# Optimization experiments

Measured on AMD Instinct MI355X. Metric: run time of the kernel, lower is better.

The kernel has to match this reference:

```python
import jax, jax.numpy as jnp
import numpy as np

NUM_HEADS = 4
FEAT_DIM = 128
EMBED_DIM = 128
B, K, C, H, W = 2, 8, 128, 128, 128


def _cross_attn(Qf, Kf, Vf, qw, qb, kw, kb, aqw, aqb, akw, akb):
    """Faithful port of PixelCrossAttentionRefiner._cross_attn.
    Qf: [B, Cq, H, W]; Kf: [B, K, Ck, H, W]; Vf: [B, K, C, H, W].
    Uses only the (head-averaged) softmax weights of MultiheadAttention,
    L2-renormalizes them, then takes a weighted sum of RAW values.
    """
    b, _, h, w = Qf.shape
    k_cand = Kf.shape[1]
    bn = b * h * w
    # Query: per-pixel feature vector -> q1 projection -> attn in-proj (query part)
    Query = jnp.transpose(Qf, (0, 2, 3, 1)).reshape(bn, -1)            # [BN, Cq]
    q = Query @ qw.T + qb                                               # [BN, E]
    # Key: NOTE torch does .permute(0,1,3,4,2).reshape(B*N, K, -1) which is a
    # flat row-major reinterpretation of the (B,K,H,W,Ck) buffer; jnp reshape
    # after transpose has identical semantics, so this is bit-faithful.
    Key = jnp.transpose(Kf, (0, 1, 3, 4, 2)).reshape(bn, k_cand, -1)    # [BN, K, Ck]
    kk = Key @ kw.T + kb                                                # [BN, K, E]
    # nn.MultiheadAttention internal in-projections (value path is dead code)
    qa = q @ aqw.T + aqb                                                # [BN, E]
    ka = kk @ akw.T + akb                                               # [BN, K, E]
    e = qa.shape[-1]
    dh = e // NUM_HEADS
    qh = qa.reshape(bn, NUM_HEADS, dh)
    kh = ka.reshape(bn, k_cand, NUM_HEADS, dh)
    scale = 1.0 / np.sqrt(dh).astype(np.float32)
    scores = jnp.einsum('mhd,mkhd->mhk', qh, kh) * scale                # [BN, H, K]
    attw = jax.nn.softmax(scores, axis=-1).mean(axis=1)                 # avg heads -> [BN, K]
    # F.normalize(p=2, dim=-1, eps=1e-12)
    attw = attw / jnp.maximum(jnp.linalg.norm(attw, axis=-1, keepdims=True), 1e-12)
    Value = jnp.transpose(Vf, (0, 1, 3, 4, 2)).reshape(bn, k_cand, -1)  # [BN, K, C]
    out = jnp.einsum('mk,mkc->mc', attw, Value)                         # [BN, C]
    return jnp.transpose(out.reshape(b, h, w, -1), (0, 3, 1, 2))        # [B, C, H, W]


def _forward(HF_star, HF_cands, Z_cands,
             q1_w, q1_b, k1_w, k1_b, a1_qw, a1_qb, a1_kw, a1_kb,
             q2_w, q2_b, k2_w, k2_b, a2_qw, a2_qb, a2_kw, a2_kb):
    b, c, h, w = HF_star.shape
    k_cand = HF_cands.shape[1]
    i = jnp.linspace(0.0, 1.0, h, dtype=HF_star.dtype)
    j = jnp.linspace(0.0, 1.0, w, dtype=HF_star.dtype)
    ig, jg = jnp.meshgrid(i, j, indexing='ij')
    ig = jnp.broadcast_to(ig[None, None], (b, 1, h, w))
    jg = jnp.broadcast_to(jg[None, None], (b, 1, h, w))
    Q1 = jnp.concatenate([HF_star, ig, jg], axis=1)                     # [B, C+2, H, W]
    ik = jnp.broadcast_to(ig[:, None], (b, k_cand, 1, h, w))
    jk = jnp.broadcast_to(jg[:, None], (b, k_cand, 1, h, w))
    K1 = jnp.concatenate([HF_cands, ik, jk], axis=2)                    # [B, K, C+2, H, W]
    z_star = _cross_attn(Q1, K1, Z_cands, q1_w, q1_b, k1_w, k1_b,
                         a1_qw, a1_qb, a1_kw, a1_kb)                    # [B, C, H, W]
    z_exp = jnp.broadcast_to(z_star[:, None], (b, k_cand, c, h, w))
    Q2 = jnp.concatenate([HF_star, z_star, ig, jg], axis=1)             # [B, 2C+2, H, W]
    K2 = jnp.concatenate([HF_cands, z_exp, ik, jk], axis=2)             # [B, K, 2C+2, H, W]
    z_hat = _cross_attn(Q2, K2, Z_cands, q2_w, q2_b, k2_w, k2_b,
                        a2_qw, a2_qb, a2_kw, a2_kb)
    return z_star, z_hat


def setup_inputs() -> dict:
    key = jax.random.key(0)
    ks = jax.random.split(key, 16)
    E = EMBED_DIM
    d1 = FEAT_DIM + 2
    d2 = 2 * FEAT_DIM + 2

    def lin(k, fan_out, fan_in):
        bound = 1.0 / np.sqrt(fan_in)
        kw, kb = jax.random.split(k)
        return (jax.random.uniform(kw, (fan_out, fan_in), jnp.float32, -bound, bound),
                jax.random.uniform(kb, (fan_out,), jnp.float32, -bound, bound))

    q1_w, q1_b = lin(ks[0], E, d1)
    k1_w, k1_b = lin(ks[1], E, d1)
    q2_w, q2_b = lin(ks[2], E, d2)
    k2_w, k2_b = lin(ks[3], E, d2)
    a1_qw, a1_qb = lin(ks[4], E, E)
    a1_kw, a1_kb = lin(ks[5], E, E)
    a2_qw, a2_qb = lin(ks[6], E, E)
    a2_kw, a2_kb = lin(ks[7], E, E)
    return {
        'HF_star': jax.random.normal(ks[8], (B, C, H, W), jnp.float32),
        'HF_cands': jax.random.normal(ks[9], (B, K, C, H, W), jnp.float32),
        'Z_cands': jax.random.normal(ks[10], (B, K, C, H, W), jnp.float32),
        'q1_w': q1_w, 'q1_b': q1_b, 'k1_w': k1_w, 'k1_b': k1_b,
        'a1_qw': a1_qw, 'a1_qb': a1_qb, 'a1_kw': a1_kw, 'a1_kb': a1_kb,
        'q2_w': q2_w, 'q2_b': q2_b, 'k2_w': k2_w, 'k2_b': k2_b,
        'a2_qw': a2_qw, 'a2_qb': a2_qb, 'a2_kw': a2_kw, 'a2_kb': a2_kb,
    }


def reference(HF_star, HF_cands, Z_cands,
              q1_w, q1_b, k1_w, k1_b, a1_qw, a1_qb, a1_kw, a1_kb,
              q2_w, q2_b, k2_w, k2_b, a2_qw, a2_qb, a2_kw, a2_kb):
    return _forward(HF_star, HF_cands, Z_cands,
                    q1_w, q1_b, k1_w, k1_b, a1_qw, a1_qb, a1_kw, a1_kb,
                    q2_w, q2_b, k2_w, k2_b, a2_qw, a2_qb, a2_kw, a2_kb)
```

## Files before the change

kernel.cpp:

```cpp
#include <hip/hip_runtime.h>
#include <math.h>

constexpr int Bc = 2, Kc = 8, HWc = 16384;
constexpr float SCALE  = 0.17677669529663687f;
constexpr float INV127 = 1.0f / 127.0f;

using short8 = __attribute__((ext_vector_type(8))) short;
using f32x4  = __attribute__((ext_vector_type(4))) float;

constexpr int OWQ1 = 0;
constexpr int OBQ1 = OWQ1 + 130 * 128;
constexpr int OWK1 = OBQ1 + 128;
constexpr int OBK1 = OWK1 + 130 * 128;
constexpr int OWQ2 = OBK1 + 128;
constexpr int OBQ2 = OWQ2 + 258 * 128;
constexpr int OWK2 = OBQ2 + 128;
constexpr int OBK2 = OWK2 + 258 * 128;
constexpr int OPACK = OBK2 + 128;
constexpr int PQ1 = 0;
constexpr int PQ2 = PQ1 + 32 * 512;
constexpr int PY1 = PQ2 + 64 * 512;
constexpr int PY2 = PY1 + 32 * 512;

__device__ __forceinline__ unsigned bfpack(float a, float b) {
    unsigned ua = __float_as_uint(a); ua = (ua + 0x7FFFu + ((ua >> 16) & 1u)) >> 16;
    unsigned ub = __float_as_uint(b); ub = (ub + 0x7FFFu + ((ub >> 16) & 1u)) >> 16;
    return ua | (ub << 16);
}
__device__ __forceinline__ short bf1(float a) {
    unsigned ua = __float_as_uint(a); ua = (ua + 0x7FFFu + ((ua >> 16) & 1u)) >> 16;
    return (short)ua;
}
__device__ __forceinline__ float bflo(unsigned u) { return __uint_as_float(u << 16); }
__device__ __forceinline__ float bfhi(unsigned u) { return __uint_as_float(u & 0xFFFF0000u); }
__device__ __forceinline__ float bf2f(short s) {
    return __uint_as_float(((unsigned)(unsigned short)s) << 16);
}

__global__ __launch_bounds__(128) void prep_kernel(
    const float* __restrict__ q1w, const float* __restrict__ q1b,
    const float* __restrict__ k1w, const float* __restrict__ k1b,
    const float* __restrict__ a1qw, const float* __restrict__ a1qb,
    const float* __restrict__ a1kw, const float* __restrict__ a1kb,
    const float* __restrict__ q2w, const float* __restrict__ q2b,
    const float* __restrict__ k2w, const float* __restrict__ k2b,
    const float* __restrict__ a2qw, const float* __restrict__ a2qb,
    const float* __restrict__ a2kw, const float* __restrict__ a2kb,
    float* __restrict__ ws)
{
    const int job = blockIdx.x / 260;
    const int d   = blockIdx.x % 260;
    const float *aw, *ab, *w, *wb;
    float *owt, *ob;
    int D;
    if (job == 0)      { aw=a1qw; ab=a1qb; w=q1w; wb=q1b; owt=ws+OWQ1; ob=ws+OBQ1; D=130; }
    else if (job == 1) { aw=a1kw; ab=a1kb; w=k1w; wb=k1b; owt=ws+OWK1; ob=ws+OBK1; D=130; }
    else if (job == 2) { aw=a2qw; ab=a2qb; w=q2w; wb=q2b; owt=ws+OWQ2; ob=ws+OBQ2; D=258; }
    else               { aw=a2kw; ab=a2kb; w=k2w; wb=k2b; owt=ws+OWK2; ob=ws+OBK2; D=258; }
    const int e = threadIdx.x;
    if (d < D) {
        float acc = 0.f;
        for (int f = 0; f < 128; ++f) acc += aw[e * 128 + f] * w[f * D + d];
        owt[d * 128 + e] = acc;
    } else if (d == D) {
        float acc = ab[e];
        for (int f = 0; f < 128; ++f) acc += aw[e * 128 + f] * wb[f];
        ob[e] = acc;
    }
}

__global__ __launch_bounds__(64) void pack_kernel(float* __restrict__ ws)
{
    short* pk = (short*)(ws + OPACK);
    const int l = threadIdx.x, bid = blockIdx.x;
    const float* w;
    short* dst;
    short v[8];
    if (bid < 32) {
        const int et = bid >> 2, kt = bid & 3;
        w = ws + OWQ1;
        dst = pk + PQ1 + ((size_t)(et * 4 + kt) * 64 + l) * 8;
        #pragma unroll
        for (int idx = 0; idx < 8; ++idx)
            v[idx] = bf1(w[(kt * 32 + (l >> 4) * 8 + idx) * 128 + et * 16 + (l & 15)]);
    } else if (bid < 96) {
        const int b2 = bid - 32, et = b2 >> 3, kt = b2 & 7;
        w = ws + OWQ2;
        dst = pk + PQ2 + ((size_t)(et * 8 + kt) * 64 + l) * 8;
        #pragma unroll
        for (int idx = 0; idx < 8; ++idx)
            v[idx] = bf1(w[(kt * 32 + (l >> 4) * 8 + idx) * 128 + et * 16 + (l & 15)]);
    } else if (bid < 128) {
        const int b2 = bid - 96, ct = b2 >> 2, h = b2 & 3;
        w = ws + OWK1;
        dst = pk + PY1 + ((size_t)(ct * 4 + h) * 64 + l) * 8;
        #pragma unroll
        for (int idx = 0; idx < 8; ++idx)
            v[idx] = bf1(w[(ct * 16 + (l & 15)) * 128 + h * 32 + (l >> 4) * 8 + idx]);
    } else {
        const int b2 = bid - 128, ct = b2 >> 2, h = b2 & 3;
        w = ws + OWK2;
        dst = pk + PY2 + ((size_t)(ct * 4 + h) * 64 + l) * 8;
        #pragma unroll
        for (int idx = 0; idx < 8; ++idx)
            v[idx] = bf1(w[(ct * 16 + (l & 15)) * 128 + h * 32 + (l >> 4) * 8 + idx]);
    }
    uint4 u;
    u.x = (unsigned)(unsigned short)v[0] | ((unsigned)(unsigned short)v[1] << 16);
    u.y = (unsigned)(unsigned short)v[2] | ((unsigned)(unsigned short)v[3] << 16);
    u.z = (unsigned)(unsigned short)v[4] | ((unsigned)(unsigned short)v[5] << 16);
    u.w = (unsigned)(unsigned short)v[6] | ((unsigned)(unsigned short)v[7] << 16);
    *(uint4*)dst = u;
}

template <int STAGE>
__global__ __launch_bounds__(256) void stage_kernel(
    const float* __restrict__ HFs,
    const float* __restrict__ HFc,
    const float* __restrict__ Zc,
    const float* __restrict__ ws,
    const float* __restrict__ zst,
    float* __restrict__ out)
{
    constexpr int CQ  = (STAGE == 1) ? 128 : 256;
    constexpr int CK  = CQ;
    constexpr int NP  = CK / 128;
    constexpr int NKT = CQ / 32;

    const float* qwt = ws + ((STAGE == 1) ? OWQ1 : OWQ2);
    const float* qb_ = ws + ((STAGE == 1) ? OBQ1 : OBQ2);
    const float* kwt = ws + ((STAGE == 1) ? OWK1 : OWK2);
    const float* kb_ = ws + ((STAGE == 1) ? OBK1 : OBK2);
    const short* pk  = (const short*)(ws + OPACK);
    const short* aQ  = pk + ((STAGE == 1) ? PQ1 : PQ2);
    const short* aY  = pk + ((STAGE == 1) ? PY1 : PY2);

    __shared__ __align__(16) char smem[27136];
    short* sXF = (short*)smem;
    uint2* sYQ = (uint2*)smem;
    short* sQF = (short*)(smem + 17408);
    float* sYX = (float*)(smem + 21504);
    float* sHW = sYX + 192;
    float* sSc = sHW + 576;
    float* sAW = sSc + 512;

    const int t   = threadIdx.x;
    const int l   = t & 63;
    const int wv  = t >> 6;
    const int bid = blockIdx.x;
    const int b   = bid >> 10;
    const int rem = bid & 1023;
    const int ks  = rem >> 7;
    const int hp  = rem & 127;
    const int r0  = ks * 2048 + hp * 16;

    const float ik = (float)hp * INV127;
    const float iq = (float)(r0 >> 7) * INV127;
    const int   w0 = r0 & 127;

    {
        const int q = t & 15, cq = t >> 4;
        #pragma unroll
        for (int r = 0; r < CQ / 64; ++r) {
            const int c0 = cq * 4 + r * 64;
            const float* src = (STAGE == 1 || c0 < 128)
                ? HFs + ((size_t)(b * 128 + c0)) * HWc + r0 + q
                : zst + ((size_t)(b * 128 + (c0 - 128))) * HWc + r0 + q;
            const float x0 = src[0];
            const float x1 = src[(size_t)HWc];
            const float x2 = src[(size_t)2 * HWc];
            const float x3 = src[(size_t)3 * HWc];
            uint2 u; u.x = bfpack(x0, x1); u.y = bfpack(x2, x3);
            const int kt = c0 >> 5, g = (c0 & 31) >> 3, idx0 = c0 & 7;
            *(uint2*)&sXF[kt * 512 + (q + 16 * g) * 8 + idx0] = u;
        }
    }
    __syncthreads();

    {
        const float jqv = (float)(w0 + (l & 15)) * INV127;
        f32x4 acc0, acc1;
        #pragma unroll
        for (int r = 0; r < 4; ++r) {
            const int e0 = (wv * 2 + 0) * 16 + (l >> 4) * 4 + r;
            const int e1 = (wv * 2 + 1) * 16 + (l >> 4) * 4 + r;
            acc0[r] = qb_[e0] + iq * qwt[(size_t)CQ * 128 + e0]
                             + jqv * qwt[(size_t)(CQ + 1) * 128 + e0];
            acc1[r] = qb_[e1] + iq * qwt[(size_t)CQ * 128 + e1]
                             + jqv * qwt[(size_t)(CQ + 1) * 128 + e1];
        }
        #pragma unroll
        for (int kt = 0; kt < NKT; ++kt) {
            const short8 bfr = *(const short8*)&sXF[kt * 512 + l * 8];
            const short8 a0 = *(const short8*)&aQ[(((wv * 2 + 0) * NKT + kt) * 64 + l) * 8];
            const short8 a1 = *(const short8*)&aQ[(((wv * 2 + 1) * NKT + kt) * 64 + l) * 8];
            acc0 = __builtin_amdgcn_mfma_f32_16x16x32_bf16(a0, bfr, acc0, 0, 0, 0);
            acc1 = __builtin_amdgcn_mfma_f32_16x16x32_bf16(a1, bfr, acc1, 0, 0, 0);
        }
        #pragma unroll
        for (int m = 0; m < 2; ++m) {
            const f32x4 a = m ? acc1 : acc0;
            const int e0 = (wv * 2 + m) * 16 + (l >> 4) * 4;
            const int kt = e0 >> 5, g = (e0 & 31) >> 3, idx0 = e0 & 7;
            uint2 u; u.x = bfpack(a[0], a[1]); u.y = bfpack(a[2], a[3]);
            *(uint2*)&sQF[kt * 512 + ((l & 15) + 16 * g) * 8 + idx0] = u;
        }
    }
    __syncthreads();

    if (t < 192) {
        const int q = t & 15, h = (t >> 4) & 3, which = t >> 6;
        const float* wrow = (which == 0) ? kwt + (size_t)CK * 128
                          : (which == 1) ? kwt + (size_t)(CK + 1) * 128
                                         : kb_;
        float acc = 0.f;
        #pragma unroll
        for (int e32 = 0; e32 < 32; ++e32) {
            const int e2 = h * 32 + e32;
            const int g = (e2 & 31) >> 3, idx = e2 & 7;
            acc += wrow[e2] * bf2f(sQF[h * 512 + (q + 16 * g) * 8 + idx]);
        }
        sYX[(which * 4 + h) * 16 + q] = acc;
    }

    short8 bq0 = *(const short8*)&sQF[0 * 512 + l * 8];
    short8 bq1 = *(const short8*)&sQF[1 * 512 + l * 8];
    short8 bq2 = *(const short8*)&sQF[2 * 512 + l * 8];
    short8 bq3 = *(const short8*)&sQF[3 * 512 + l * 8];

    float sacc[4] = {0.f, 0.f, 0.f, 0.f};
    const int pos = t & 127;
    const int ch  = t >> 7;
    const int q   = pos >> 3;
    const f32x4 zf = {0.f, 0.f, 0.f, 0.f};

    #pragma unroll
    for (int p = 0; p < NP; ++p) {
        #pragma unroll
        for (int m = 0; m < 2; ++m) {
            const int ctl = wv * 2 + m;
            const int ct  = p * 8 + ctl;
            f32x4 d0, d1, d2, d3;
            {
                const short8 a0 = *(const short8*)&aY[(((ct * 4) + 0) * 64 + l) * 8];
                const short8 a1 = *(const short8*)&aY[(((ct * 4) + 1) * 64 + l) * 8];
                const short8 a2 = *(const short8*)&aY[(((ct * 4) + 2) * 64 + l) * 8];
                const short8 a3 = *(const short8*)&aY[(((ct * 4) + 3) * 64 + l) * 8];
                d0 = __builtin_amdgcn_mfma_f32_16x16x32_bf16(a0, bq0, zf, 0, 0, 0);
                d1 = __builtin_amdgcn_mfma_f32_16x16x32_bf16(a1, bq1, zf, 0, 0, 0);
                d2 = __builtin_amdgcn_mfma_f32_16x16x32_bf16(a2, bq2, zf, 0, 0, 0);
                d3 = __builtin_amdgcn_mfma_f32_16x16x32_bf16(a3, bq3, zf, 0, 0, 0);
            }
            #pragma unroll
            for (int r = 0; r < 4; ++r) {
                const int cl = ctl * 16 + (l >> 4) * 4 + r;
                uint2 u;
                u.x = bfpack(d0[r], d1[r]);
                u.y = bfpack(d2[r], d3[r]);
                sYQ[cl * 17 + (l & 15)] = u;
            }
        }
        __syncthreads();

        {
            const int cs = p * 128 + ch * 64;
            const float* xp = (STAGE == 1 || cs < 128)
                ? HFc + (((size_t)(b * Kc + ks)) * 128 + cs) * HWc + hp * 128 + pos
                : zst + ((size_t)(b * 128 + (cs - 128))) * HWc + hp * 128 + pos;
            const uint2* yqp = &sYQ[(ch * 64) * 17 + q];
            #pragma unroll 8
            for (int cc = 0; cc < 64; ++cc) {
                const float x = xp[(size_t)cc * HWc];
                const uint2 u = yqp[cc * 17];
                sacc[0] += x * bflo(u.x); sacc[1] += x * bfhi(u.x);
                sacc[2] += x * bflo(u.y); sacc[3] += x * bfhi(u.y);
            }
        }
        __syncthreads();
    }

    if (ch == 1) {
        #pragma unroll
        for (int h = 0; h < 4; ++h) sHW[pos * 4 + h] = sacc[h];
    }
    __syncthreads();
    if (t < 128) {
        const float jk = (float)pos * INV127;
        #pragma unroll
        for (int h = 0; h < 4; ++h) {
            const float s = sacc[h] + sHW[pos * 4 + h]
                          + ik * sYX[(0 * 4 + h) * 16 + q]
                          + jk * sYX[(1 * 4 + h) * 16 + q]
                          +      sYX[(2 * 4 + h) * 16 + q];
            sSc[h * 128 + pos] = s * SCALE;
        }
    }
    __syncthreads();

    if (t < 64) {
        const int qq = t & 15, h = t >> 4;
        float sc[8], m = -INFINITY;
        #pragma unroll
        for (int j = 0; j < 8; ++j) {
            sc[j] = sSc[h * 128 + qq * 8 + j];
            m = fmaxf(m, sc[j]);
        }
        float sum = 0.f;
        #pragma unroll
        for (int j = 0; j < 8; ++j) { sc[j] = __expf(sc[j] - m); sum += sc[j]; }
        const float inv = 0.25f / sum;
        #pragma unroll
        for (int j = 0; j < 8; ++j) sHW[(h * 16 + qq) * 9 + j] = sc[j] * inv;
    }
    __syncthreads();
    if (t < 16) {
        float at[8];
        float n2 = 0.f;
        #pragma unroll
        for (int j = 0; j < 8; ++j) {
            at[j] = sHW[(0 * 16 + t) * 9 + j] + sHW[(1 * 16 + t) * 9 + j]
                  + sHW[(2 * 16 + t) * 9 + j] + sHW[(3 * 16 + t) * 9 + j];
            n2 += at[j] * at[j];
        }
        const float nrm = fmaxf(sqrtf(n2), 1e-12f);
        #pragma unroll
        for (int j = 0; j < 8; ++j) sAW[t * 8 + j] = at[j] / nrm;
    }
    __syncthreads();

    {
        const int idx = t & 15, cg = t >> 4;
        const int c8  = cg * 8;
        const float4 a0 = *(const float4*)&sAW[idx * 8];
        const float4 a1 = *(const float4*)&sAW[idx * 8 + 4];
        const float* zb = Zc + (((size_t)(b * Kc + ks)) * 128 + c8) * HWc + hp * 128 + idx * 8;
        float* ob = out + ((size_t)(b * 128 + c8)) * HWc + r0 + idx;
        #pragma unroll
        for (int i = 0; i < 8; ++i) {
            const float4 z0 = *(const float4*)(zb + (size_t)i * HWc);
            const float4 z1 = *(const float4*)(zb + (size_t)i * HWc + 4);
            ob[(size_t)i * HWc] =
                a0.x * z0.x + a0.y * z0.y + a0.z * z0.z + a0.w * z0.w +
                a1.x * z1.x + a1.y * z1.y + a1.z * z1.z + a1.w * z1.w;
        }
    }
}

extern "C" void kernel_launch(void* const* d_in, const int* in_sizes, int n_in,
                              void* d_out, int out_size, void* d_ws, size_t ws_size,
                              hipStream_t stream)
{
    const float* HFs = (const float*)d_in[0];
    const float* HFc = (const float*)d_in[1];
    const float* Zc  = (const float*)d_in[2];
    float* ws    = (float*)d_ws;
    float* zstar = (float*)d_out;
    float* zhat  = zstar + (size_t)Bc * 128 * HWc;

    prep_kernel<<<1040, 128, 0, stream>>>(
        (const float*)d_in[3],  (const float*)d_in[4],
        (const float*)d_in[5],  (const float*)d_in[6],
        (const float*)d_in[7],  (const float*)d_in[8],
        (const float*)d_in[9],  (const float*)d_in[10],
        (const float*)d_in[11], (const float*)d_in[12],
        (const float*)d_in[13], (const float*)d_in[14],
        (const float*)d_in[15], (const float*)d_in[16],
        (const float*)d_in[17], (const float*)d_in[18],
        ws);

    pack_kernel<<<192, 64, 0, stream>>>(ws);

    stage_kernel<1><<<2048, 256, 0, stream>>>(HFs, HFc, Zc, ws, zstar, zstar);
    stage_kernel<2><<<2048, 256, 0, stream>>>(HFs, HFc, Zc, ws, zstar, zhat);
}
```

Measured before the change: 151.5 us.

## Vectorize feature loads with float4 and register-tile the key-score reduction

The query feature staging now loads float4 along the pixel axis and scatters bf16 values into the MFMA layout, replacing four strided scalar loads per thread. The key-feature dot-product loop is remapped so each thread covers 4 pixels × 4 heads over 16 channels using float4 loads. Partial sums are then combined with a cross-lane shuffle plus a shared-memory reduction across waves. This cuts global load instruction count and improves reuse of each LDS read, at the cost of more registers and extra reduction steps.

```diff
diff --git a/kernel.cpp b/kernel.cpp
--- a/kernel.cpp
+++ b/kernel.cpp
@@ -138,6 +138,7 @@
     __shared__ __align__(16) char smem[27136];
     short* sXF = (short*)smem;
     uint2* sYQ = (uint2*)smem;
+    float* sRed = (float*)smem;
     short* sQF = (short*)(smem + 17408);
     float* sYX = (float*)(smem + 21504);
     float* sHW = sYX + 192;
@@ -159,20 +160,20 @@
     const int   w0 = r0 & 127;
 
     {
-        const int q = t & 15, cq = t >> 4;
+        const int qg = t & 3, c = t >> 2;
         #pragma unroll
         for (int r = 0; r < CQ / 64; ++r) {
-            const int c0 = cq * 4 + r * 64;
-            const float* src = (STAGE == 1 || c0 < 128)
-                ? HFs + ((size_t)(b * 128 + c0)) * HWc + r0 + q
-                : zst + ((size_t)(b * 128 + (c0 - 128))) * HWc + r0 + q;
-            const float x0 = src[0];
-            const float x1 = src[(size_t)HWc];
-            const float x2 = src[(size_t)2 * HWc];
-            const float x3 = src[(size_t)3 * HWc];
-            uint2 u; u.x = bfpack(x0, x1); u.y = bfpack(x2, x3);
-            const int kt = c0 >> 5, g = (c0 & 31) >> 3, idx0 = c0 & 7;
-            *(uint2*)&sXF[kt * 512 + (q + 16 * g) * 8 + idx0] = u;
+            const int cc = c + r * 64;
+            const float* src = (STAGE == 1 || cc < 128)
+                ? HFs + ((size_t)(b * 128 + cc)) * HWc + r0 + qg * 4
+                : zst + ((size_t)(b * 128 + (cc - 128))) * HWc + r0 + qg * 4;
+            const float4 x = *(const float4*)src;
+            const int kt = cc >> 5, g = (cc & 31) >> 3, idx = cc & 7;
+            short* dstb = &sXF[kt * 512 + idx + 16 * g * 8];
+            dstb[(qg * 4 + 0) * 8] = bf1(x.x);
+            dstb[(qg * 4 + 1) * 8] = bf1(x.y);
+            dstb[(qg * 4 + 2) * 8] = bf1(x.z);
+            dstb[(qg * 4 + 3) * 8] = bf1(x.w);
         }
     }
     __syncthreads();
@@ -228,10 +229,14 @@
     short8 bq2 = *(const short8*)&sQF[2 * 512 + l * 8];
     short8 bq3 = *(const short8*)&sQF[3 * 512 + l * 8];
 
-    float sacc[4] = {0.f, 0.f, 0.f, 0.f};
-    const int pos = t & 127;
-    const int ch  = t >> 7;
-    const int q   = pos >> 3;
+    const int pg = t & 31;
+    const int cs = t >> 5;
+    const int q  = pg >> 1;
+    float acc[4][4];
+    #pragma unroll
+    for (int h = 0; h < 4; ++h)
+        #pragma unroll
+        for (int j = 0; j < 4; ++j) acc[h][j] = 0.f;
     const f32x4 zf = {0.f, 0.f, 0.f, 0.f};
 
     #pragma unroll
@@ -263,35 +268,56 @@
         __syncthreads();
 
         {
-            const int cs = p * 128 + ch * 64;
-            const float* xp = (STAGE == 1 || cs < 128)
-                ? HFc + (((size_t)(b * Kc + ks)) * 128 + cs) * HWc + hp * 128 + pos
-                : zst + ((size_t)(b * 128 + (cs - 128))) * HWc + hp * 128 + pos;
-            const uint2* yqp = &sYQ[(ch * 64) * 17 + q];
+            const int cbase = p * 128 + cs * 16;
+            const float* xp = (STAGE == 1 || cbase < 128)
+                ? HFc + (((size_t)(b * Kc + ks)) * 128 + cbase) * HWc + hp * 128 + pg * 4
+                : zst + ((size_t)(b * 128 + (cbase - 128))) * HWc + hp * 128 + pg * 4;
+            const uint2* yqp = &sYQ[(cs * 16) * 17 + q];
             #pragma unroll 8
-            for (int cc = 0; cc < 64; ++cc) {
-                const float x = xp[(size_t)cc * HWc];
+            for (int cc = 0; cc < 16; ++cc) {
+                const float4 x = *(const float4*)(xp + (size_t)cc * HWc);
                 const uint2 u = yqp[cc * 17];
-                sacc[0] += x * bflo(u.x); sacc[1] += x * bfhi(u.x);
-                sacc[2] += x * bflo(u.y); sacc[3] += x * bfhi(u.y);
+                const float y0 = bflo(u.x), y1 = bfhi(u.x);
+                const float y2 = bflo(u.y), y3 = bfhi(u.y);
+                acc[0][0] += y0 * x.x; acc[0][1] += y0 * x.y;
+                acc[0][2] += y0 * x.z; acc[0][3] += y0 * x.w;
+                acc[1][0] += y1 * x.x; acc[1][1] += y1 * x.y;
+                acc[1][2] += y1 * x.z; acc[1][3] += y1 * x.w;
+                acc[2][0] += y2 * x.x; acc[2][1] += y2 * x.y;
+                acc[2][2] += y2 * x.z; acc[2][3] += y2 * x.w;
+                acc[3][0] += y3 * x.x; acc[3][1] += y3 * x.y;
+                acc[3][2] += y3 * x.z; acc[3][3] += y3 * x.w;
             }
         }
         __syncthreads();
     }
 
-    if (ch == 1) {
-        #pragma unroll
-        for (int h = 0; h < 4; ++h) sHW[pos * 4 + h] = sacc[h];
-    }
-    __syncthreads();
+    #pragma unroll
+    for (int h = 0; h < 4; ++h)
+        #pragma unroll
+        for (int j = 0; j < 4; ++j)
+            acc[h][j] += __shfl_xor(acc[h][j], 32, 64);
+    if (l < 32) {
+        #pragma unroll
+        for (int h = 0; h < 4; ++h)
+            #pragma unroll
+            for (int j = 0; j < 4; ++j)
+                sRed[wv * 512 + pg * 16 + h * 4 + j] = acc[h][j];
+    }
+    __syncthreads();
+
     if (t < 128) {
+        const int pos = t, pgg = pos >> 2, j = pos & 3, qq = pos >> 3;
         const float jk = (float)pos * INV127;
         #pragma unroll
         for (int h = 0; h < 4; ++h) {
-            const float s = sacc[h] + sHW[pos * 4 + h]
-                          + ik * sYX[(0 * 4 + h) * 16 + q]
-                          + jk * sYX[(1 * 4 + h) * 16 + q]
-                          +      sYX[(2 * 4 + h) * 16 + q];
+            const float v = sRed[0 * 512 + pgg * 16 + h * 4 + j]
+                          + sRed[1 * 512 + pgg * 16 + h * 4 + j]
+                          + sRed[2 * 512 + pgg * 16 + h * 4 + j]
+                          + sRed[3 * 512 + pgg * 16 + h * 4 + j];
+            const float s = v + ik * sYX[(0 * 4 + h) * 16 + qq]
+                              + jk * sYX[(1 * 4 + h) * 16 + qq]
+                              +      sYX[(2 * 4 + h) * 16 + qq];
             sSc[h * 128 + pos] = s * SCALE;
         }
     }
```

New measurement: 154.7 us. 2.1% more time.
